# Performance work log

Measured on AMD Instinct MI355X. Metric: run time of the kernel, lower is better.

Reference implementation:

```python
import jax, jax.numpy as jnp
import numpy as np
import math

N_AGENTS = 512
TRAJ_LEN = 16
TAU = 2048          # obs_shape + n_actions = 1536 + 512
MSG = 32768         # messages_shape
HID = 512           # args.hidden_dim
DV = MSG // N_AGENTS  # 64, per-agent message dim


def setup_inputs() -> dict:
    key = jax.random.key(0)
    ks = jax.random.split(key, 8)
    s = 0.02
    return {
        "imagined_trajectory": jax.random.normal(ks[0], (TRAJ_LEN, N_AGENTS, TAU), jnp.float32),
        "received_messages": jax.random.normal(ks[1], (N_AGENTS, MSG), jnp.float32),
        "Wq": jax.random.normal(ks[2], (MSG, HID), jnp.float32) * s,
        "bq": jnp.zeros((HID,), jnp.float32),
        "Wk": jax.random.normal(ks[3], (TAU, HID), jnp.float32) * s,
        "bk": jnp.zeros((HID,), jnp.float32),
        "Wv": jax.random.normal(ks[4], (TAU, DV), jnp.float32) * s,
        "bv": jnp.zeros((DV,), jnp.float32),
    }


def reference(imagined_trajectory, received_messages, Wq, bq, Wk, bk, Wv, bv):
    # q: [N, H]
    q = received_messages @ Wq + bq
    T, N, tau = imagined_trajectory.shape
    taus = imagined_trajectory.reshape(T * N, tau)          # row j*N + i == (traj step j, agent i)
    k = (taus @ Wk + bk).reshape(T, N, HID)                 # [T, N, H]
    v = (taus @ Wv + bv).reshape(T, N, DV)                  # [T, N, Dv]
    # per-agent dot-product attention over trajectory steps (vectorized form of
    # the original double python loop: score[i, j] = dot(q[i], k[j*N+i]) / sqrt(H))
    scores = jnp.einsum("nh,tnh->nt", q, k) / math.sqrt(HID)  # [N, T]
    alpha = jax.nn.softmax(scores, axis=-1)
    messages = jnp.einsum("nt,tnd->nd", alpha, v)           # [N, Dv]
    return messages
```

## Files before the change

kernel.cpp:

```cpp
#include <hip/hip_runtime.h>
#include <hip/hip_fp16.h>

#define N_AG 512
#define TRAJ 16
#define TAU_ 2048
#define MSG_ 32768
#define HID_ 512
#define DV_ 64
#define SPLITQ 64
#define LDS_K 40

typedef _Float16 f16x8 __attribute__((ext_vector_type(8)));
typedef _Float16 f16x4 __attribute__((ext_vector_type(4)));
typedef _Float16 f16x2 __attribute__((ext_vector_type(2)));
typedef __fp16 h16x2 __attribute__((ext_vector_type(2)));
typedef float f32x4 __attribute__((ext_vector_type(4)));

__global__ __launch_bounds__(256) void prep_wv(const float* __restrict__ Wv,
                                               _Float16* __restrict__ Wvt)
{
    __shared__ float td[64][65];
    const int k0 = blockIdx.x * 64;
    for (int e = threadIdx.x; e < 4096; e += 256) {
        const int ki = e >> 6, ni = e & 63;
        td[ki][ni] = Wv[(size_t)(k0 + ki) * DV_ + ni];
    }
    __syncthreads();
    for (int e = threadIdx.x; e < 4096; e += 256) {
        const int ni = e >> 6, ki = e & 63;
        Wvt[(size_t)ni * TAU_ + k0 + ki] = (_Float16)td[ki][ni];
    }
}

__global__ __launch_bounds__(512, 1) void qgemm(const float* __restrict__ X,
                                                const float* __restrict__ Wq,
                                                _Float16* __restrict__ qpart)
{
    __shared__ __align__(1024) char smem[65536];
    const int tid = threadIdx.x;
    const int l = tid & 63;
    const int w = tid >> 6;
    const int wr = w >> 2, wc = w & 3;
    const int r15 = l & 15;
    const int swz = ((l >> 4) ^ ((r15 >> 1) & 3)) * 16;

    const int b = blockIdx.x;
    const int sw = (b & 7) * 32 + (b >> 3);
    const int s = sw >> 2;
    const int bm = (sw >> 1) & 1;
    const int bn = sw & 1;
    const size_t ks0 = (size_t)s * 512;

    const int am = tid >> 1;
    const int ak = (tid & 1) << 4;
    const float* agp = X + (size_t)(bm * 256 + am) * MSG_ + ks0 + ak;
    const int ac0 = ak >> 3;
    const int akey = (am >> 1) & 3;
    const int aoff0 = am * 64 + ((ac0 ^ akey)) * 16;
    const int aoff1 = am * 64 + (((ac0 + 1) ^ akey)) * 16;

    const int bn_ = tid & 255;
    const int kh0 = (tid >> 8) << 4;
    const float* bgp = Wq + (size_t)(ks0 + kh0) * HID_ + bn * 256 + bn_;
    const int bc0 = kh0 >> 3;
    const int bkey = (bn_ >> 1) & 3;
    const int boff0 = bn_ * 64 + ((bc0 ^ bkey)) * 16;
    const int boff1 = bn_ * 64 + (((bc0 + 1) ^ bkey)) * 16;

    f32x4 acc[8][4];
#pragma unroll
    for (int mi = 0; mi < 8; ++mi)
#pragma unroll
        for (int ni = 0; ni < 4; ++ni)
            acc[mi][ni] = (f32x4){0.f, 0.f, 0.f, 0.f};

    struct Stage { float4 a[4]; float bb[16]; };
    Stage rA, rB;
    const int nt = 16;

    auto load_stage = [&](Stage& r, int t) {
        const float* ap = agp + t * 32;
#pragma unroll
        for (int i = 0; i < 4; ++i) r.a[i] = *(const float4*)(ap + 4 * i);
        const float* bp = bgp + (size_t)t * 32 * HID_;
#pragma unroll
        for (int i = 0; i < 16; ++i) r.bb[i] = bp[(size_t)i * HID_];
    };
    auto write_stage = [&](Stage& r, int d) {
        char* base = smem + d * 32768;
        const float* fa = (const float*)&r.a[0];
        union { h16x2 h2[4]; f16x8 v; } u0, u1;
        u0.h2[0] = __builtin_amdgcn_cvt_pkrtz(fa[0], fa[1]);
        u0.h2[1] = __builtin_amdgcn_cvt_pkrtz(fa[2], fa[3]);
        u0.h2[2] = __builtin_amdgcn_cvt_pkrtz(fa[4], fa[5]);
        u0.h2[3] = __builtin_amdgcn_cvt_pkrtz(fa[6], fa[7]);
        u1.h2[0] = __builtin_amdgcn_cvt_pkrtz(fa[8], fa[9]);
        u1.h2[1] = __builtin_amdgcn_cvt_pkrtz(fa[10], fa[11]);
        u1.h2[2] = __builtin_amdgcn_cvt_pkrtz(fa[12], fa[13]);
        u1.h2[3] = __builtin_amdgcn_cvt_pkrtz(fa[14], fa[15]);
        *(f16x8*)(base + aoff0) = u0.v;
        *(f16x8*)(base + aoff1) = u1.v;
        union { h16x2 h2[4]; f16x8 v; } v0, v1;
        v0.h2[0] = __builtin_amdgcn_cvt_pkrtz(r.bb[0], r.bb[1]);
        v0.h2[1] = __builtin_amdgcn_cvt_pkrtz(r.bb[2], r.bb[3]);
        v0.h2[2] = __builtin_amdgcn_cvt_pkrtz(r.bb[4], r.bb[5]);
        v0.h2[3] = __builtin_amdgcn_cvt_pkrtz(r.bb[6], r.bb[7]);
        v1.h2[0] = __builtin_amdgcn_cvt_pkrtz(r.bb[8], r.bb[9]);
        v1.h2[1] = __builtin_amdgcn_cvt_pkrtz(r.bb[10], r.bb[11]);
        v1.h2[2] = __builtin_amdgcn_cvt_pkrtz(r.bb[12], r.bb[13]);
        v1.h2[3] = __builtin_amdgcn_cvt_pkrtz(r.bb[14], r.bb[15]);
        *(f16x8*)(base + 16384 + boff0) = v0.v;
        *(f16x8*)(base + 16384 + boff1) = v1.v;
    };
    auto compute = [&](int d) {
        const char* ab = smem + d * 32768;
        const char* bb = smem + d * 32768 + 16384;
        f16x8 af[8], bf[4];
#pragma unroll
        for (int mi = 0; mi < 8; ++mi)
            af[mi] = *(const f16x8*)(ab + (wr * 128 + mi * 16 + r15) * 64 + swz);
#pragma unroll
        for (int ni = 0; ni < 4; ++ni)
            bf[ni] = *(const f16x8*)(bb + (wc * 64 + ni * 16 + r15) * 64 + swz);
#pragma unroll
        for (int mi = 0; mi < 8; ++mi)
#pragma unroll
            for (int ni = 0; ni < 4; ++ni)
                acc[mi][ni] = __builtin_amdgcn_mfma_f32_16x16x32_f16(
                    af[mi], bf[ni], acc[mi][ni], 0, 0, 0);
    };

    load_stage(rA, 0);
    load_stage(rB, 1);
    write_stage(rA, 0);
    __syncthreads();
    for (int t = 0; t < nt; t += 2) {
        if (t + 2 < nt) load_stage(rA, t + 2);
        compute(0);
        if (t + 1 < nt) write_stage(rB, 1);
        __syncthreads();
        if (t + 3 < nt) load_stage(rB, t + 3);
        compute(1);
        if (t + 2 < nt) write_stage(rA, 0);
        __syncthreads();
    }

    _Float16* cp = qpart + (size_t)s * (N_AG * HID_);
#pragma unroll
    for (int mi = 0; mi < 8; ++mi)
#pragma unroll
        for (int ni = 0; ni < 4; ++ni) {
            const int row = bm * 256 + wr * 128 + mi * 16 + ((l >> 4) << 2);
            const int col = bn * 256 + wc * 64 + ni * 16 + r15;
#pragma unroll
            for (int r = 0; r < 4; ++r)
                cp[(size_t)(row + r) * HID_ + col] = (_Float16)acc[mi][ni][r];
        }
}

__global__ __launch_bounds__(256) void qreduce(const _Float16* __restrict__ qpart,
                                               const float* __restrict__ bq,
                                               float* __restrict__ q)
{
    const int e = blockIdx.x * 512 + threadIdx.x * 2;
    float a0 = bq[e & (HID_ - 1)], a1 = bq[(e + 1) & (HID_ - 1)];
#pragma unroll
    for (int s = 0; s < SPLITQ; ++s) {
        f16x2 p = *(const f16x2*)(qpart + (size_t)s * (N_AG * HID_) + e);
        a0 += (float)p[0];
        a1 += (float)p[1];
    }
    q[e] = a0;
    q[e + 1] = a1;
}

__global__ __launch_bounds__(256, 4) void qkgemm(const float* __restrict__ q,
                                                 const float* __restrict__ Wk,
                                                 _Float16* __restrict__ qk)
{
    __shared__ __align__(16) _Float16 smem[4 * 64 * LDS_K];
    _Float16* As = smem;
    _Float16* Bs = smem + 2 * 64 * LDS_K;
    const int tid = threadIdx.x;
    const int lane = tid & 63;
    const int wid = tid >> 6;
    const int wr = wid >> 1;
    const int wc = wid & 1;
    const int r15 = lane & 15;
    const int kblk = (lane >> 4) << 3;

    const int b = blockIdx.x;
    const int w = (b & 7) * 32 + (b >> 3);
    const int bm = w >> 5;
    const int bn = w & 31;

    const bool isB = tid >= 128;
    const int rt = tid & 127;
    const int srow = rt >> 1;
    const int skh = (rt & 1) << 4;
    const float* gp = (isB ? Wk + (size_t)(bn * 64) * HID_ : q + (size_t)(bm * 64) * HID_)
                      + (size_t)srow * HID_ + skh;
    _Float16* lbase = (isB ? Bs : As) + srow * LDS_K + skh;

    f32x4 acc[2][2];
#pragma unroll
    for (int mi = 0; mi < 2; ++mi)
#pragma unroll
        for (int ni = 0; ni < 2; ++ni)
            acc[mi][ni] = (f32x4){0.f, 0.f, 0.f, 0.f};

    float4 rA[4], rB[4];
    auto load_stage = [&](float4 (&r)[4], int ks) {
#pragma unroll
        for (int i = 0; i < 4; ++i) r[i] = *(const float4*)(gp + ks + 4 * i);
    };
    auto write_stage = [&](float4 (&r)[4], int buf) {
        const float* f = (const float*)&r[0];
        f16x8 h0, h1;
#pragma unroll
        for (int i = 0; i < 8; ++i) { h0[i] = (_Float16)f[i]; h1[i] = (_Float16)f[8 + i]; }
        *(f16x8*)(lbase + buf * 64 * LDS_K) = h0;
        *(f16x8*)(lbase + buf * 64 * LDS_K + 8) = h1;
    };
    auto compute = [&](int buf) {
        const _Float16* ab = As + buf * 64 * LDS_K;
        const _Float16* bbp = Bs + buf * 64 * LDS_K;
        f16x8 af[2], bf[2];
#pragma unroll
        for (int mi = 0; mi < 2; ++mi)
            af[mi] = *(const f16x8*)(ab + (wr * 32 + mi * 16 + r15) * LDS_K + kblk);
#pragma unroll
        for (int ni = 0; ni < 2; ++ni)
            bf[ni] = *(const f16x8*)(bbp + (wc * 32 + ni * 16 + r15) * LDS_K + kblk);
#pragma unroll
        for (int mi = 0; mi < 2; ++mi)
#pragma unroll
            for (int ni = 0; ni < 2; ++ni)
                acc[mi][ni] = __builtin_amdgcn_mfma_f32_16x16x32_f16(
                    af[mi], bf[ni], acc[mi][ni], 0, 0, 0);
    };

    load_stage(rA, 0);
    load_stage(rB, 32);
    write_stage(rA, 0);
    __syncthreads();
    for (int t = 0; t < 16; t += 2) {
        if (t + 2 < 16) load_stage(rA, (t + 2) << 5);
        compute(0);
        if (t + 1 < 16) write_stage(rB, 1);
        __syncthreads();
        if (t + 3 < 16) load_stage(rB, (t + 3) << 5);
        compute(1);
        if (t + 2 < 16) write_stage(rA, 0);
        __syncthreads();
    }
#pragma unroll
    for (int mi = 0; mi < 2; ++mi)
#pragma unroll
        for (int ni = 0; ni < 2; ++ni) {
            const int row = bm * 64 + wr * 32 + mi * 16 + ((lane >> 4) << 2);
            const int col = bn * 64 + wc * 32 + ni * 16 + r15;
#pragma unroll
            for (int r = 0; r < 4; ++r)
                qk[(size_t)(row + r) * TAU_ + col] = (_Float16)acc[mi][ni][r];
        }
}

__global__ __launch_bounds__(256, 2) void svmix(const float* __restrict__ traj,
                                                const _Float16* __restrict__ qkm,
                                                _Float16* __restrict__ wmixg)
{
    const int n = blockIdx.x;
    const int tid = threadIdx.x;
    const int w = tid >> 6;
    const int l = tid & 63;
    __shared__ _Float16 tl[TRAJ][TAU_];
    __shared__ float scrw[4][TRAJ];
    __shared__ float scr[TRAJ];

    const int c0 = tid * 8;
    f16x8 q8 = *(const f16x8*)(qkm + (size_t)n * TAU_ + c0);

#pragma unroll
    for (int t = 0; t < TRAJ; ++t) {
        const float* tr = traj + ((size_t)(t * N_AG + n)) * TAU_ + c0;
        float4 x0 = *(const float4*)(tr);
        float4 x1 = *(const float4*)(tr + 4);
        union { h16x2 h2[4]; f16x8 v; } u;
        u.h2[0] = __builtin_amdgcn_cvt_pkrtz(x0.x, x0.y);
        u.h2[1] = __builtin_amdgcn_cvt_pkrtz(x0.z, x0.w);
        u.h2[2] = __builtin_amdgcn_cvt_pkrtz(x1.x, x1.y);
        u.h2[3] = __builtin_amdgcn_cvt_pkrtz(x1.z, x1.w);
        *(f16x8*)(&tl[t][c0]) = u.v;
        float p = x0.x * (float)q8[0] + x0.y * (float)q8[1]
                + x0.z * (float)q8[2] + x0.w * (float)q8[3]
                + x1.x * (float)q8[4] + x1.y * (float)q8[5]
                + x1.z * (float)q8[6] + x1.w * (float)q8[7];
#pragma unroll
        for (int off = 32; off > 0; off >>= 1) p += __shfl_xor(p, off);
        if (l == 0) scrw[w][t] = p;
    }
    __syncthreads();
    if (tid < TRAJ)
        scr[tid] = scrw[0][tid] + scrw[1][tid] + scrw[2][tid] + scrw[3][tid];
    __syncthreads();

    const float inv = 0.04419417382415922f;
    float sv[TRAJ];
    float mx = -1e30f;
#pragma unroll
    for (int t = 0; t < TRAJ; ++t) { sv[t] = scr[t] * inv; mx = fmaxf(mx, sv[t]); }
    float ssum = 0.f;
#pragma unroll
    for (int t = 0; t < TRAJ; ++t) { sv[t] = expf(sv[t] - mx); ssum += sv[t]; }
    const float rs = 1.f / ssum;
#pragma unroll
    for (int t = 0; t < TRAJ; ++t) sv[t] *= rs;

    float o[8] = {0.f, 0.f, 0.f, 0.f, 0.f, 0.f, 0.f, 0.f};
#pragma unroll
    for (int t = 0; t < TRAJ; ++t) {
        f16x8 t8 = *(const f16x8*)(&tl[t][c0]);
#pragma unroll
        for (int i = 0; i < 8; ++i) o[i] += sv[t] * (float)t8[i];
    }
    f16x8 ho;
#pragma unroll
    for (int i = 0; i < 8; ++i) ho[i] = (_Float16)o[i];
    *(f16x8*)(wmixg + (size_t)n * TAU_ + c0) = ho;
}

__global__ __launch_bounds__(256) void outgemm(const _Float16* __restrict__ wmixg,
                                               const _Float16* __restrict__ Wvt,
                                               const float* __restrict__ bv,
                                               float* __restrict__ out)
{
    const int a0 = blockIdx.x * 8;
    const int tid = threadIdx.x;
    __shared__ _Float16 wl[8][TAU_];
    __shared__ float pls[4][8][64];

#pragma unroll
    for (int i = 0; i < 8; ++i) {
        const int slot = i * 256 + tid;
        const int row = slot >> 8;
        const int col = (slot & 255) * 8;
        *(f16x8*)(&wl[row][col]) = *(const f16x8*)(wmixg + (size_t)(a0 + row) * TAU_ + col);
    }
    __syncthreads();

    const int j = tid & 63;
    const int qh = tid >> 6;
    float pacc[8] = {0.f, 0.f, 0.f, 0.f, 0.f, 0.f, 0.f, 0.f};
    const _Float16* wv = Wvt + (size_t)j * TAU_ + qh * 512;
    for (int k = 0; k < 512; k += 8) {
        f16x8 w8 = *(const f16x8*)(wv + k);
        float wf[8];
#pragma unroll
        for (int i = 0; i < 8; ++i) wf[i] = (float)w8[i];
#pragma unroll
        for (int a = 0; a < 8; ++a) {
            f16x8 t8 = *(const f16x8*)(&wl[a][qh * 512 + k]);
#pragma unroll
            for (int i = 0; i < 8; ++i) pacc[a] += wf[i] * (float)t8[i];
        }
    }
#pragma unroll
    for (int a = 0; a < 8; ++a) pls[qh][a][j] = pacc[a];
    __syncthreads();

#pragma unroll
    for (int oo = 0; oo < 2; ++oo) {
        const int o = oo * 256 + tid;
        const int a = o >> 6, jj = o & 63;
        out[(size_t)(a0 + a) * DV_ + jj] =
            pls[0][a][jj] + pls[1][a][jj] + pls[2][a][jj] + pls[3][a][jj] + bv[jj];
    }
}

extern "C" void kernel_launch(void* const* d_in, const int* in_sizes, int n_in,
                              void* d_out, int out_size, void* d_ws, size_t ws_size,
                              hipStream_t stream)
{
    const float* traj = (const float*)d_in[0];
    const float* msgs = (const float*)d_in[1];
    const float* Wq   = (const float*)d_in[2];
    const float* bq   = (const float*)d_in[3];
    const float* Wk   = (const float*)d_in[4];
    const float* bk   = (const float*)d_in[5];
    const float* Wv   = (const float*)d_in[6];
    const float* bv   = (const float*)d_in[7];
    float* out = (float*)d_out;
    (void)bk;

    _Float16* qpart = (_Float16*)d_ws;
    float*    q     = (float*)(qpart + (size_t)SPLITQ * N_AG * HID_);
    _Float16* qk    = (_Float16*)(q + (size_t)N_AG * HID_);
    _Float16* Wvt   = qk + (size_t)N_AG * TAU_;
    _Float16* wmixg = Wvt + (size_t)DV_ * TAU_;

    prep_wv<<<32, 256, 0, stream>>>(Wv, Wvt);
    qgemm<<<256, 512, 0, stream>>>(msgs, Wq, qpart);
    qreduce<<<512, 256, 0, stream>>>(qpart, bq, q);
    qkgemm<<<256, 256, 0, stream>>>(q, Wk, qk);
    svmix<<<512, 256, 0, stream>>>(traj, qk, wmixg);
    outgemm<<<64, 256, 0, stream>>>(wmixg, Wvt, bv, out);
}
```

Measured before the change: 93.43 us.

## Pre-transpose Wq to fp16 and stream it into LDS via direct DMA

A new kernel transposes Wq to an fp16 K-major layout on every call. The q GEMM then loads its B tiles with global_load_lds direct-to-LDS copies instead of strided scalar fp32 loads followed by conversion. The GEMM also moves from double to triple buffering with explicit vmcnt and lgkmcnt waits and raises MFMA priority during compute. The cost is an extra full pass over the 64MB Wq (read fp32, write fp16) on each call. The transposed buffer aliases later workspace, so prep_wv is moved after the q reduction.

Measured after the change: 125.2 us. 34.0% more time.

```diff
diff --git a/kernel.cpp b/kernel.cpp
--- a/kernel.cpp
+++ b/kernel.cpp
@@ -16,6 +16,33 @@
 typedef __fp16 h16x2 __attribute__((ext_vector_type(2)));
 typedef float f32x4 __attribute__((ext_vector_type(4)));
 
+#define VMCNT(n) asm volatile("s_waitcnt vmcnt(" #n ")" ::: "memory")
+#define LGKM0    asm volatile("s_waitcnt lgkmcnt(0)" ::: "memory")
+#define BAR()    __builtin_amdgcn_s_barrier()
+
+__device__ __forceinline__ void gload16(const void* g, void* l) {
+    __builtin_amdgcn_global_load_lds(
+        (const __attribute__((address_space(1))) void*)g,
+        (__attribute__((address_space(3))) void*)l, 16, 0, 0);
+}
+
+__global__ __launch_bounds__(256) void prep_wq(const float* __restrict__ Wq,
+                                               _Float16* __restrict__ Wqt)
+{
+    __shared__ float td[64][65];
+    const int k0 = blockIdx.x * 64;
+    const int n0 = blockIdx.y * 64;
+    for (int e = threadIdx.x; e < 4096; e += 256) {
+        const int ki = e >> 6, ni = e & 63;
+        td[ki][ni] = Wq[(size_t)(k0 + ki) * HID_ + n0 + ni];
+    }
+    __syncthreads();
+    for (int e = threadIdx.x; e < 4096; e += 256) {
+        const int ni = e >> 6, ki = e & 63;
+        Wqt[(size_t)(n0 + ni) * MSG_ + k0 + ki] = (_Float16)td[ki][ni];
+    }
+}
+
 __global__ __launch_bounds__(256) void prep_wv(const float* __restrict__ Wv,
                                                _Float16* __restrict__ Wvt)
 {
@@ -32,11 +59,11 @@
     }
 }
 
-__global__ __launch_bounds__(512, 1) void qgemm(const float* __restrict__ X,
-                                                const float* __restrict__ Wq,
+__global__ __launch_bounds__(512, 2) void qgemm(const float* __restrict__ X,
+                                                const _Float16* __restrict__ Wqt,
                                                 _Float16* __restrict__ qpart)
 {
-    __shared__ __align__(1024) char smem[65536];
+    __shared__ __align__(1024) char smem[98304];
     const int tid = threadIdx.x;
     const int l = tid & 63;
     const int w = tid >> 6;
@@ -59,13 +86,10 @@
     const int aoff0 = am * 64 + ((ac0 ^ akey)) * 16;
     const int aoff1 = am * 64 + (((ac0 + 1) ^ akey)) * 16;
 
-    const int bn_ = tid & 255;
-    const int kh0 = (tid >> 8) << 4;
-    const float* bgp = Wq + (size_t)(ks0 + kh0) * HID_ + bn * 256 + bn_;
-    const int bc0 = kh0 >> 3;
-    const int bkey = (bn_ >> 1) & 3;
-    const int boff0 = bn_ * 64 + ((bc0 ^ bkey)) * 16;
-    const int boff1 = bn_ * 64 + (((bc0 + 1) ^ bkey)) * 16;
+    const int bsrcc = (l & 3) ^ ((l >> 3) & 3);
+    const _Float16* bgp = Wqt + (size_t)(bn * 256 + w * 32 + (l >> 2)) * MSG_
+                          + ks0 + bsrcc * 8;
+    const int bld0 = (w * 32) * 64;
 
     f32x4 acc[8][4];
 #pragma unroll
@@ -74,21 +98,16 @@
         for (int ni = 0; ni < 4; ++ni)
             acc[mi][ni] = (f32x4){0.f, 0.f, 0.f, 0.f};
 
-    struct Stage { float4 a[4]; float bb[16]; };
-    Stage rA, rB;
-    const int nt = 16;
-
-    auto load_stage = [&](Stage& r, int t) {
-        const float* ap = agp + t * 32;
-#pragma unroll
-        for (int i = 0; i < 4; ++i) r.a[i] = *(const float4*)(ap + 4 * i);
-        const float* bp = bgp + (size_t)t * 32 * HID_;
-#pragma unroll
-        for (int i = 0; i < 16; ++i) r.bb[i] = bp[(size_t)i * HID_];
-    };
-    auto write_stage = [&](Stage& r, int d) {
+    float4 r0[4], r1[4], r2[4];
+
+    auto aload = [&](float4 (&r)[4], int t) {
+        const float* p = agp + t * 32;
+#pragma unroll
+        for (int i = 0; i < 4; ++i) r[i] = *(const float4*)(p + 4 * i);
+    };
+    auto awrite = [&](float4 (&r)[4], int d) {
         char* base = smem + d * 32768;
-        const float* fa = (const float*)&r.a[0];
+        const float* fa = (const float*)&r[0];
         union { h16x2 h2[4]; f16x8 v; } u0, u1;
         u0.h2[0] = __builtin_amdgcn_cvt_pkrtz(fa[0], fa[1]);
         u0.h2[1] = __builtin_amdgcn_cvt_pkrtz(fa[2], fa[3]);
@@ -100,17 +119,12 @@
         u1.h2[3] = __builtin_amdgcn_cvt_pkrtz(fa[14], fa[15]);
         *(f16x8*)(base + aoff0) = u0.v;
         *(f16x8*)(base + aoff1) = u1.v;
-        union { h16x2 h2[4]; f16x8 v; } v0, v1;
-        v0.h2[0] = __builtin_amdgcn_cvt_pkrtz(r.bb[0], r.bb[1]);
-        v0.h2[1] = __builtin_amdgcn_cvt_pkrtz(r.bb[2], r.bb[3]);
-        v0.h2[2] = __builtin_amdgcn_cvt_pkrtz(r.bb[4], r.bb[5]);
-        v0.h2[3] = __builtin_amdgcn_cvt_pkrtz(r.bb[6], r.bb[7]);
-        v1.h2[0] = __builtin_amdgcn_cvt_pkrtz(r.bb[8], r.bb[9]);
-        v1.h2[1] = __builtin_amdgcn_cvt_pkrtz(r.bb[10], r.bb[11]);
-        v1.h2[2] = __builtin_amdgcn_cvt_pkrtz(r.bb[12], r.bb[13]);
-        v1.h2[3] = __builtin_amdgcn_cvt_pkrtz(r.bb[14], r.bb[15]);
-        *(f16x8*)(base + 16384 + boff0) = v0.v;
-        *(f16x8*)(base + 16384 + boff1) = v1.v;
+    };
+    auto bdma = [&](int t, int d) {
+        char* base = smem + d * 32768 + 16384 + bld0;
+        const _Float16* gp = bgp + (size_t)t * 32;
+        gload16(gp, base);
+        gload16(gp + (size_t)16 * MSG_, base + 1024);
     };
     auto compute = [&](int d) {
         const char* ab = smem + d * 32768;
@@ -122,28 +136,51 @@
 #pragma unroll
         for (int ni = 0; ni < 4; ++ni)
             bf[ni] = *(const f16x8*)(bb + (wc * 64 + ni * 16 + r15) * 64 + swz);
+        __builtin_amdgcn_s_setprio(1);
 #pragma unroll
         for (int mi = 0; mi < 8; ++mi)
 #pragma unroll
             for (int ni = 0; ni < 4; ++ni)
                 acc[mi][ni] = __builtin_amdgcn_mfma_f32_16x16x32_f16(
                     af[mi], bf[ni], acc[mi][ni], 0, 0, 0);
-    };
-
-    load_stage(rA, 0);
-    load_stage(rB, 1);
-    write_stage(rA, 0);
-    __syncthreads();
-    for (int t = 0; t < nt; t += 2) {
-        if (t + 2 < nt) load_stage(rA, t + 2);
-        compute(0);
-        if (t + 1 < nt) write_stage(rB, 1);
-        __syncthreads();
-        if (t + 3 < nt) load_stage(rB, t + 3);
-        compute(1);
-        if (t + 2 < nt) write_stage(rA, 0);
-        __syncthreads();
-    }
+        __builtin_amdgcn_s_setprio(0);
+    };
+
+    bdma(0, 0); aload(r0, 0);
+    bdma(1, 1); aload(r1, 1);
+    bdma(2, 2); aload(r2, 2);
+    VMCNT(12);
+    awrite(r0, 0);
+    LGKM0; BAR();
+
+#define QSTEP(T, B0, RB, RW, B1)                       \
+    compute(B0); BAR();                                \
+    bdma((T) + 3, B0); aload(RB, (T) + 3);             \
+    VMCNT(12);                                         \
+    awrite(RW, B1);                                    \
+    LGKM0; BAR();
+
+    for (int g = 0; g < 4; ++g) {
+        const int t = g * 3;
+        QSTEP(t + 0, 0, r0, r1, 1)
+        QSTEP(t + 1, 1, r1, r2, 2)
+        QSTEP(t + 2, 2, r2, r0, 0)
+    }
+#undef QSTEP
+    compute(0); BAR();
+    bdma(15, 0); aload(r0, 15);
+    VMCNT(12);
+    awrite(r1, 1);
+    LGKM0; BAR();
+    compute(1); BAR();
+    VMCNT(6);
+    awrite(r2, 2);
+    LGKM0; BAR();
+    compute(2); BAR();
+    VMCNT(0);
+    awrite(r0, 0);
+    LGKM0; BAR();
+    compute(0);
 
     _Float16* cp = qpart + (size_t)s * (N_AG * HID_);
 #pragma unroll
@@ -395,13 +432,15 @@
 
     _Float16* qpart = (_Float16*)d_ws;
     float*    q     = (float*)(qpart + (size_t)SPLITQ * N_AG * HID_);
-    _Float16* qk    = (_Float16*)(q + (size_t)N_AG * HID_);
+    _Float16* Wqt   = (_Float16*)(q + (size_t)N_AG * HID_);
+    _Float16* qk    = Wqt;
     _Float16* Wvt   = qk + (size_t)N_AG * TAU_;
     _Float16* wmixg = Wvt + (size_t)DV_ * TAU_;
 
+    prep_wq<<<dim3(512, 8), 256, 0, stream>>>(Wq, Wqt);
+    qgemm<<<256, 512, 0, stream>>>(msgs, Wqt, qpart);
+    qreduce<<<512, 256, 0, stream>>>(qpart, bq, q);
     prep_wv<<<32, 256, 0, stream>>>(Wv, Wvt);
-    qgemm<<<256, 512, 0, stream>>>(msgs, Wq, qpart);
-    qreduce<<<512, 256, 0, stream>>>(qpart, bq, q);
     qkgemm<<<256, 256, 0, stream>>>(q, Wk, qk);
     svmix<<<512, 256, 0, stream>>>(traj, qk, wmixg);
     outgemm<<<64, 256, 0, stream>>>(wmixg, Wvt, bv, out);
```

## Double split-K for Q GEMM, vectorize reductions and reuse workspace

Applied to the files above, without the earlier changes.

Doubles the split-K factor of the Q projection GEMM from 64 to 128 slices. Each block now handles half the K range and the grid grows to 512 blocks with two blocks allowed per CU, which is meant to improve occupancy and latency hiding. The reduce kernel now uses 8-wide f16 loads and float4 stores, and prep_wv writes packed 8-half vectors. The qk buffer reuses the qpart workspace, which is why prep_wv is launched after qreduce. The trade-off is twice as many fp16 partials to write and reduce, and launch_bounds(512,2) may force register spills for the 128-float accumulator.

After: 112.2 us. 20.1% more time.

```diff
diff --git a/kernel.cpp b/kernel.cpp
--- a/kernel.cpp
+++ b/kernel.cpp
@@ -7,7 +7,7 @@
 #define MSG_ 32768
 #define HID_ 512
 #define DV_ 64
-#define SPLITQ 64
+#define SPLITQ 128
 #define LDS_K 40
 
 typedef _Float16 f16x8 __attribute__((ext_vector_type(8)));
@@ -26,13 +26,18 @@
         td[ki][ni] = Wv[(size_t)(k0 + ki) * DV_ + ni];
     }
     __syncthreads();
-    for (int e = threadIdx.x; e < 4096; e += 256) {
-        const int ni = e >> 6, ki = e & 63;
-        Wvt[(size_t)ni * TAU_ + k0 + ki] = (_Float16)td[ki][ni];
-    }
-}
-
-__global__ __launch_bounds__(512, 1) void qgemm(const float* __restrict__ X,
+#pragma unroll
+    for (int p = 0; p < 2; ++p) {
+        const int u = p * 256 + threadIdx.x;
+        const int ni = u >> 3, kj = (u & 7) * 8;
+        f16x8 h;
+#pragma unroll
+        for (int i = 0; i < 8; ++i) h[i] = (_Float16)td[kj + i][ni];
+        *(f16x8*)(Wvt + (size_t)ni * TAU_ + k0 + kj) = h;
+    }
+}
+
+__global__ __launch_bounds__(512, 2) void qgemm(const float* __restrict__ X,
                                                 const float* __restrict__ Wq,
                                                 _Float16* __restrict__ qpart)
 {
@@ -45,11 +50,11 @@
     const int swz = ((l >> 4) ^ ((r15 >> 1) & 3)) * 16;
 
     const int b = blockIdx.x;
-    const int sw = (b & 7) * 32 + (b >> 3);
+    const int sw = (b & 7) * 64 + (b >> 3);
     const int s = sw >> 2;
     const int bm = (sw >> 1) & 1;
     const int bn = sw & 1;
-    const size_t ks0 = (size_t)s * 512;
+    const size_t ks0 = (size_t)s * 256;
 
     const int am = tid >> 1;
     const int ak = (tid & 1) << 4;
@@ -76,7 +81,7 @@
 
     struct Stage { float4 a[4]; float bb[16]; };
     Stage rA, rB;
-    const int nt = 16;
+    const int nt = 8;
 
     auto load_stage = [&](Stage& r, int t) {
         const float* ap = agp + t * 32;
@@ -162,16 +167,19 @@
                                                const float* __restrict__ bq,
                                                float* __restrict__ q)
 {
-    const int e = blockIdx.x * 512 + threadIdx.x * 2;
-    float a0 = bq[e & (HID_ - 1)], a1 = bq[(e + 1) & (HID_ - 1)];
+    const int e = (blockIdx.x * 256 + threadIdx.x) * 8;
+    const int h0 = e & (HID_ - 1);
+    float a[8];
+#pragma unroll
+    for (int i = 0; i < 8; ++i) a[i] = bq[h0 + i];
 #pragma unroll
     for (int s = 0; s < SPLITQ; ++s) {
-        f16x2 p = *(const f16x2*)(qpart + (size_t)s * (N_AG * HID_) + e);
-        a0 += (float)p[0];
-        a1 += (float)p[1];
-    }
-    q[e] = a0;
-    q[e + 1] = a1;
+        f16x8 p = *(const f16x8*)(qpart + (size_t)s * (N_AG * HID_) + e);
+#pragma unroll
+        for (int i = 0; i < 8; ++i) a[i] += (float)p[i];
+    }
+    *(float4*)(q + e)     = (float4){a[0], a[1], a[2], a[3]};
+    *(float4*)(q + e + 4) = (float4){a[4], a[5], a[6], a[7]};
 }
 
 __global__ __launch_bounds__(256, 4) void qkgemm(const float* __restrict__ q,
@@ -395,13 +403,13 @@
 
     _Float16* qpart = (_Float16*)d_ws;
     float*    q     = (float*)(qpart + (size_t)SPLITQ * N_AG * HID_);
-    _Float16* qk    = (_Float16*)(q + (size_t)N_AG * HID_);
+    _Float16* qk    = qpart;
     _Float16* Wvt   = qk + (size_t)N_AG * TAU_;
     _Float16* wmixg = Wvt + (size_t)DV_ * TAU_;
 
+    qgemm<<<512, 512, 0, stream>>>(msgs, Wq, qpart);
+    qreduce<<<128, 256, 0, stream>>>(qpart, bq, q);
     prep_wv<<<32, 256, 0, stream>>>(Wv, Wvt);
-    qgemm<<<256, 512, 0, stream>>>(msgs, Wq, qpart);
-    qreduce<<<512, 256, 0, stream>>>(qpart, bq, q);
     qkgemm<<<256, 256, 0, stream>>>(q, Wk, qk);
     svmix<<<512, 256, 0, stream>>>(traj, qk, wmixg);
     outgemm<<<64, 256, 0, stream>>>(wmixg, Wvt, bv, out);
```
